# Optimization experiments

Measured on AMD Instinct MI355X. Metric: run time of the kernel, lower is better.

## Reference

```python
import jax, jax.numpy as jnp
import numpy as np

IN_SIZE = 1024
CLASSES = 7
N = 50000
LN_EPS = 1e-5


def _chain(x, w, b, g, beta):
    # Linear -> (Dropout=identity at eval) -> LayerNorm -> GELU(exact erf)
    h = x @ w.T + b
    mu = jnp.mean(h, axis=-1, keepdims=True)
    var = jnp.var(h, axis=-1, keepdims=True)
    h = (h - mu) / jnp.sqrt(var + LN_EPS) * g + beta
    return jax.nn.gelu(h, approximate=False)


def setup_inputs() -> dict:
    key = jax.random.key(0)
    ks = jax.random.split(key, 16)
    d = IN_SIZE
    std = 1.0 / np.sqrt(d)
    inp = {
        "features": jax.random.normal(ks[0], (N, d), jnp.float32),
        "c": jax.random.normal(ks[1], (N, CLASSES), jnp.float32),
        "key_w": jax.random.uniform(ks[2], (d, d), jnp.float32, -std, std),
        "key_b": jax.random.uniform(ks[3], (d,), jnp.float32, -std, std),
        "key_g": jnp.ones((d,), jnp.float32),
        "key_beta": jnp.zeros((d,), jnp.float32),
        "query_w": jax.random.uniform(ks[4], (d, d), jnp.float32, -std, std),
        "query_b": jax.random.uniform(ks[5], (d,), jnp.float32, -std, std),
        "query_g": jnp.ones((d,), jnp.float32),
        "query_beta": jnp.zeros((d,), jnp.float32),
        "value_w": jax.random.uniform(ks[6], (d, d), jnp.float32, -std, std),
        "value_b": jax.random.uniform(ks[7], (d,), jnp.float32, -std, std),
        "value_g": jnp.ones((d,), jnp.float32),
        "value_beta": jnp.zeros((d,), jnp.float32),
        "head_w": jax.random.uniform(ks[8], (CLASSES, CLASSES, d), jnp.float32, -1.0 / np.sqrt(CLASSES * d), 1.0 / np.sqrt(CLASSES * d)),
        "head_b": jax.random.uniform(ks[9], (CLASSES,), jnp.float32, -1.0 / np.sqrt(CLASSES * d), 1.0 / np.sqrt(CLASSES * d)),
    }
    return inp


def reference(features, c, key_w, key_b, key_g, key_beta,
              query_w, query_b, query_g, query_beta,
              value_w, value_b, value_g, value_beta,
              head_w, head_b):
    K = _chain(features, key_w, key_b, key_g, key_beta)          # [N, d]
    V = _chain(K, value_w, value_b, value_g, value_beta)         # [N, d]
    Q = _chain(K, query_w, query_b, query_g, query_beta)         # [N, d]
    # critical (top-scoring) instance per class
    top_idx = jnp.argmax(c, axis=0)                              # [classes]
    m_feats = K[top_idx]                                         # [classes, d]
    q_max = _chain(m_feats, query_w, query_b, query_g, query_beta)  # [classes, d]
    A = Q @ q_max.T                                              # [N, classes]
    A = jax.nn.softmax(A / jnp.sqrt(jnp.float32(Q.shape[1])), axis=0)
    B = A.T @ V                                                  # [classes, d]
    # Conv1d(classes, classes, kernel_size=d) on [1, classes, d] -> full contraction
    C = jnp.einsum('ik,oik->o', B, head_w) + head_b              # [classes]
    C = C.reshape(1, -1)
    return (C, A, B.reshape(1, CLASSES, -1))
```

## Files before the change

kernel.cpp:

```cpp
#include <hip/hip_runtime.h>


typedef unsigned short u16;
typedef __attribute__((ext_vector_type(8))) short          bf16x8;
typedef __attribute__((ext_vector_type(8))) unsigned short u16x8;
typedef __attribute__((ext_vector_type(4))) unsigned short u16x4;
typedef __attribute__((ext_vector_type(4))) float          f32x4;

#define DDIM  1024
#define NROWS 50000
#define MP    50048
#define NCLS  7
#define MPD4  12512

__device__ __forceinline__ u16 f2bf(float f) {
  unsigned u = __float_as_uint(f);
  u = (u + 0x7FFFu + ((u >> 16) & 1u)) >> 16;
  return (u16)u;
}
__device__ __forceinline__ float bf2f(u16 h) {
  return __uint_as_float(((unsigned)h) << 16);
}
__device__ __forceinline__ float gelu(float x) {
  return 0.5f * x * (1.0f + erff(x * 0.70710678118654752f));
}

__device__ __forceinline__ void load16_lds(const u16* g, u16* l) {
  __builtin_amdgcn_global_load_lds(
      (const __attribute__((address_space(1))) unsigned int*)(const void*)g,
      (__attribute__((address_space(3))) unsigned int*)(void*)l, 16, 0, 0);
}

__global__ __launch_bounds__(256) void k_convert(const float* __restrict__ src,
                                                 u16* __restrict__ dst,
                                                 int rows_total, int rows_valid) {
  const size_t total = (size_t)rows_total * DDIM / 8;
  const size_t stride = (size_t)gridDim.x * blockDim.x;
  for (size_t i = (size_t)blockIdx.x * blockDim.x + threadIdx.x; i < total; i += stride) {
    const size_t e = i * 8;
    const int row = (int)(e >> 10);
    u16x8 o = {0, 0, 0, 0, 0, 0, 0, 0};
    if (row < rows_valid) {
      const float4* p = (const float4*)(src + e);
      float4 f0 = p[0], f1 = p[1];
      o[0] = f2bf(f0.x); o[1] = f2bf(f0.y); o[2] = f2bf(f0.z); o[3] = f2bf(f0.w);
      o[4] = f2bf(f1.x); o[5] = f2bf(f1.y); o[6] = f2bf(f1.z); o[7] = f2bf(f1.w);
    }
    *(u16x8*)(dst + e) = o;
  }
}

__global__ __launch_bounds__(256) void k_convw(const float* __restrict__ kw,
                                               const float* __restrict__ vw,
                                               const float* __restrict__ qw,
                                               u16* __restrict__ Wk,
                                               u16* __restrict__ Wvq) {
  const int w = blockIdx.x >> 7;
  const int b = blockIdx.x & 127;
  const float* src = (w == 0) ? kw : (w == 1) ? vw : qw;
  u16* dst = (w == 0) ? Wk : (Wvq + (size_t)(w - 1) * DDIM * DDIM);
  for (int i = b * 256 + threadIdx.x; i < DDIM * DDIM / 8; i += 128 * 256) {
    const float4* p = (const float4*)(src + (size_t)i * 8);
    float4 f0 = p[0], f1 = p[1];
    u16x8 o;
    o[0] = f2bf(f0.x); o[1] = f2bf(f0.y); o[2] = f2bf(f0.z); o[3] = f2bf(f0.w);
    o[4] = f2bf(f1.x); o[5] = f2bf(f1.y); o[6] = f2bf(f1.z); o[7] = f2bf(f1.w);
    *(u16x8*)(dst + (size_t)i * 8) = o;
  }
}

__global__ __launch_bounds__(256) void k_gemm_bt(const u16* __restrict__ A,
                                                 const u16* __restrict__ B,
                                                 u16* __restrict__ C,
                                                 int lnn, int ldc) {
  __shared__ __align__(16) u16 As[4][4096];
  __shared__ __align__(16) u16 Bs[4][4096];
  const int tid  = threadIdx.x;
  const int lane = tid & 63;
  const int cpx = gridDim.x >> 3;
  const int v   = (blockIdx.x & 7) * cpx + (blockIdx.x >> 3);
  const int m0 = (v >> lnn) * 128;
  const int n0 = (v & ((1 << lnn) - 1)) * 128;
  const int wid = tid >> 6;
  const int wr = (wid >> 1) * 64;
  const int wc = (wid & 1) * 64;

  const int rA = tid >> 2;
  const int cA = (tid & 3) * 8;
  const u16* Ap0 = A + (size_t)(m0 + rA) * DDIM + cA;
  const u16* Ap1 = Ap0 + (size_t)64 * DDIM;
  const u16* Bp0 = B + (size_t)(n0 + rA) * DDIM + cA;
  const u16* Bp1 = Bp0 + (size_t)64 * DDIM;
  const int wb8 = wid * 512;

  f32x4 acc[4][4] = {};
  const int fr = lane & 15;
  const int kh = (lane >> 4) * 8;

#define STAGE_KT(KT) do { const int _b = (KT) & 3; const int _ko = (KT) * 32;  \
    load16_lds(Ap0 + _ko, &As[_b][wb8]);                                       \
    load16_lds(Ap1 + _ko, &As[_b][wb8 + 2048]);                                \
    load16_lds(Bp0 + _ko, &Bs[_b][wb8]);                                       \
    load16_lds(Bp1 + _ko, &Bs[_b][wb8 + 2048]); } while (0)

#define COMPUTE_KT(KT) do { const int _b = (KT) & 3;                           \
    const u16* _Ab = &As[_b][0]; const u16* _Bb = &Bs[_b][0];                  \
    bf16x8 a[4], b[4];                                                         \
    _Pragma("unroll") for (int i = 0; i < 4; ++i)                              \
      a[i] = *(const bf16x8*)&_Ab[(wr + i * 16 + fr) * 32 + kh];               \
    _Pragma("unroll") for (int j = 0; j < 4; ++j)                              \
      b[j] = *(const bf16x8*)&_Bb[(wc + j * 16 + fr) * 32 + kh];               \
    _Pragma("unroll") for (int i = 0; i < 4; ++i)                              \
      _Pragma("unroll") for (int j = 0; j < 4; ++j)                            \
        acc[i][j] = __builtin_amdgcn_mfma_f32_16x16x32_bf16(a[i], b[j],        \
                                                            acc[i][j], 0, 0, 0); } while (0)

  STAGE_KT(0); STAGE_KT(1); STAGE_KT(2);
  asm volatile("s_waitcnt vmcnt(8)\n\ts_barrier" ::: "memory");

#pragma unroll 4
  for (int kt = 0; kt < 28; ++kt) {
    STAGE_KT(kt + 3);
    COMPUTE_KT(kt);
    asm volatile("s_waitcnt vmcnt(8)\n\ts_barrier" ::: "memory");
  }
  STAGE_KT(31);
  COMPUTE_KT(28);
  asm volatile("s_waitcnt vmcnt(8)\n\ts_barrier" ::: "memory");
  COMPUTE_KT(29);
  asm volatile("s_waitcnt vmcnt(4)\n\ts_barrier" ::: "memory");
  COMPUTE_KT(30);
  asm volatile("s_waitcnt vmcnt(0)\n\ts_barrier" ::: "memory");
  COMPUTE_KT(31);
#undef STAGE_KT
#undef COMPUTE_KT

  const int orow = (lane >> 4) * 4;
  const int ocol = lane & 15;
#pragma unroll
  for (int i = 0; i < 4; ++i)
#pragma unroll
    for (int j = 0; j < 4; ++j) {
      const size_t base = (size_t)(m0 + wr + i * 16 + orow) * ldc + (n0 + wc + j * 16 + ocol);
#pragma unroll
      for (int r = 0; r < 4; ++r)
        C[base + (size_t)r * ldc] = f2bf(acc[i][j][r]);
    }
}

__global__ __launch_bounds__(256) void k_ln_k(const u16* __restrict__ h,
                                              const float* __restrict__ bias,
                                              const float* __restrict__ g,
                                              const float* __restrict__ beta,
                                              u16* __restrict__ out) {
  const int lane = threadIdx.x & 63;
  const int row = blockIdx.x * 4 + (threadIdx.x >> 6);
  const int c0 = lane * 8;
  u16x8* op0 = (u16x8*)(out + (size_t)row * DDIM + c0);
  u16x8* op1 = (u16x8*)(out + (size_t)row * DDIM + 512 + c0);
  if (row >= NROWS) {
    u16x8 z = {0, 0, 0, 0, 0, 0, 0, 0};
    *op0 = z; *op1 = z;
    return;
  }
  u16x8 h0 = *(const u16x8*)(h + (size_t)row * DDIM + c0);
  u16x8 h1 = *(const u16x8*)(h + (size_t)row * DDIM + 512 + c0);
  float4 a0 = *(const float4*)(bias + c0), a1 = *(const float4*)(bias + c0 + 4);
  float4 a2 = *(const float4*)(bias + 512 + c0), a3 = *(const float4*)(bias + 512 + c0 + 4);
  const float ba[8] = {a0.x, a0.y, a0.z, a0.w, a1.x, a1.y, a1.z, a1.w};
  const float bb[8] = {a2.x, a2.y, a2.z, a2.w, a3.x, a3.y, a3.z, a3.w};
  float v0[8], v1[8];
  float s1 = 0.f, s2 = 0.f;
#pragma unroll
  for (int e = 0; e < 8; ++e) {
    v0[e] = bf2f(h0[e]) + ba[e];
    v1[e] = bf2f(h1[e]) + bb[e];
    s1 += v0[e] + v1[e];
    s2 += v0[e] * v0[e] + v1[e] * v1[e];
  }
#pragma unroll
  for (int m = 1; m < 64; m <<= 1) {
    s1 += __shfl_xor(s1, m, 64);
    s2 += __shfl_xor(s2, m, 64);
  }
  const float mu = s1 * (1.0f / 1024.0f);
  const float var = s2 * (1.0f / 1024.0f) - mu * mu;
  const float rs = rsqrtf(var + 1e-5f);
  float4 g0 = *(const float4*)(g + c0), g1 = *(const float4*)(g + c0 + 4);
  float4 g2 = *(const float4*)(g + 512 + c0), g3 = *(const float4*)(g + 512 + c0 + 4);
  float4 t0 = *(const float4*)(beta + c0), t1 = *(const float4*)(beta + c0 + 4);
  float4 t2 = *(const float4*)(beta + 512 + c0), t3 = *(const float4*)(beta + 512 + c0 + 4);
  const float ga[8] = {g0.x, g0.y, g0.z, g0.w, g1.x, g1.y, g1.z, g1.w};
  const float gb[8] = {g2.x, g2.y, g2.z, g2.w, g3.x, g3.y, g3.z, g3.w};
  const float ta[8] = {t0.x, t0.y, t0.z, t0.w, t1.x, t1.y, t1.z, t1.w};
  const float tb[8] = {t2.x, t2.y, t2.z, t2.w, t3.x, t3.y, t3.z, t3.w};
  u16x8 o0, o1;
#pragma unroll
  for (int e = 0; e < 8; ++e) {
    o0[e] = f2bf(gelu((v0[e] - mu) * rs * ga[e] + ta[e]));
    o1[e] = f2bf(gelu((v1[e] - mu) * rs * gb[e] + tb[e]));
  }
  *op0 = o0; *op1 = o1;
}

__global__ __launch_bounds__(64) void k_qmax2(const float* __restrict__ argv,
                                              const int* __restrict__ argi,
                                              const u16* __restrict__ hvq,
                                              const float* __restrict__ qb,
                                              const float* __restrict__ qg,
                                              const float* __restrict__ qbeta,
                                              u16* __restrict__ qm) {
  const int j = blockIdx.x;
  const int lane = threadIdx.x;
  float bv = -3.4e38f; int bi = 0x7fffffff;
  for (int p = lane; p < 128; p += 64) {
    const float v = argv[p * NCLS + j];
    const int   i = argi[p * NCLS + j];
    if (v > bv || (v == bv && i < bi)) { bv = v; bi = i; }
  }
#pragma unroll
  for (int m = 1; m < 64; m <<= 1) {
    const float ov = __shfl_xor(bv, m, 64);
    const int   oi = __shfl_xor(bi, m, 64);
    if (ov > bv || (ov == bv && oi < bi)) { bv = ov; bi = oi; }
  }
  const int row = bi;
  const int c0 = lane * 8;
  const u16* hp = hvq + (size_t)row * 2048 + DDIM;
  u16x8 h0 = *(const u16x8*)(hp + c0);
  u16x8 h1 = *(const u16x8*)(hp + 512 + c0);
  float v0[8], v1[8];
  float s1 = 0.f, s2 = 0.f;
#pragma unroll
  for (int e = 0; e < 8; ++e) {
    v0[e] = bf2f(h0[e]) + qb[c0 + e];
    v1[e] = bf2f(h1[e]) + qb[512 + c0 + e];
    s1 += v0[e] + v1[e];
    s2 += v0[e] * v0[e] + v1[e] * v1[e];
  }
#pragma unroll
  for (int m = 1; m < 64; m <<= 1) {
    s1 += __shfl_xor(s1, m, 64);
    s2 += __shfl_xor(s2, m, 64);
  }
  const float mu = s1 * (1.0f / 1024.0f);
  const float var = s2 * (1.0f / 1024.0f) - mu * mu;
  const float rs = rsqrtf(var + 1e-5f);
  u16x8 o0, o1;
#pragma unroll
  for (int e = 0; e < 8; ++e) {
    o0[e] = f2bf(gelu((v0[e] - mu) * rs * qg[c0 + e] + qbeta[c0 + e]));
    o1[e] = f2bf(gelu((v1[e] - mu) * rs * qg[512 + c0 + e] + qbeta[512 + c0 + e]));
  }
  *(u16x8*)(qm + (size_t)j * DDIM + c0) = o0;
  *(u16x8*)(qm + (size_t)j * DDIM + 512 + c0) = o1;
}

__global__ __launch_bounds__(256) void k_ln_vq(const u16* __restrict__ h,
                                               const float* __restrict__ v_b,
                                               const float* __restrict__ v_g,
                                               const float* __restrict__ v_beta,
                                               const float* __restrict__ q_b,
                                               const float* __restrict__ q_g,
                                               const float* __restrict__ q_beta,
                                               const u16* __restrict__ qm,
                                               u16* __restrict__ V,
                                               float* __restrict__ logits) {
  __shared__ __align__(16) u16 sqm[NCLS * DDIM];
  const int tid = threadIdx.x;
  const int lane = tid & 63;
  const int half = (blockIdx.x >= MPD4) ? 1 : 0;
  const int rb = half ? (blockIdx.x - MPD4) : blockIdx.x;
  const int row = rb * 4 + (tid >> 6);
  if (half) {
    for (int i = tid; i < NCLS * DDIM / 8; i += 256)
      *(u16x8*)&sqm[i * 8] = *(const u16x8*)&qm[i * 8];
    __syncthreads();
  }
  if (row >= NROWS) return;
  const float* bias = half ? q_b : v_b;
  const float* gain = half ? q_g : v_g;
  const float* bet  = half ? q_beta : v_beta;
  const int c0 = lane * 8;
  const u16* hp = h + (size_t)row * 2048 + (size_t)half * DDIM;
  u16x8 h0 = *(const u16x8*)(hp + c0);
  u16x8 h1 = *(const u16x8*)(hp + 512 + c0);
  float4 a0 = *(const float4*)(bias + c0), a1 = *(const float4*)(bias + c0 + 4);
  float4 a2 = *(const float4*)(bias + 512 + c0), a3 = *(const float4*)(bias + 512 + c0 + 4);
  const float ba[8] = {a0.x, a0.y, a0.z, a0.w, a1.x, a1.y, a1.z, a1.w};
  const float bb[8] = {a2.x, a2.y, a2.z, a2.w, a3.x, a3.y, a3.z, a3.w};
  float v0[8], v1[8];
  float s1 = 0.f, s2 = 0.f;
#pragma unroll
  for (int e = 0; e < 8; ++e) {
    v0[e] = bf2f(h0[e]) + ba[e];
    v1[e] = bf2f(h1[e]) + bb[e];
    s1 += v0[e] + v1[e];
    s2 += v0[e] * v0[e] + v1[e] * v1[e];
  }
#pragma unroll
  for (int m = 1; m < 64; m <<= 1) {
    s1 += __shfl_xor(s1, m, 64);
    s2 += __shfl_xor(s2, m, 64);
  }
  const float mu = s1 * (1.0f / 1024.0f);
  const float var = s2 * (1.0f / 1024.0f) - mu * mu;
  const float rs = rsqrtf(var + 1e-5f);
  float4 g0 = *(const float4*)(gain + c0), g1 = *(const float4*)(gain + c0 + 4);
  float4 g2 = *(const float4*)(gain + 512 + c0), g3 = *(const float4*)(gain + 512 + c0 + 4);
  float4 t0 = *(const float4*)(bet + c0), t1 = *(const float4*)(bet + c0 + 4);
  float4 t2 = *(const float4*)(bet + 512 + c0), t3 = *(const float4*)(bet + 512 + c0 + 4);
  const float ga[8] = {g0.x, g0.y, g0.z, g0.w, g1.x, g1.y, g1.z, g1.w};
  const float gb[8] = {g2.x, g2.y, g2.z, g2.w, g3.x, g3.y, g3.z, g3.w};
  const float ta[8] = {t0.x, t0.y, t0.z, t0.w, t1.x, t1.y, t1.z, t1.w};
  const float tb[8] = {t2.x, t2.y, t2.z, t2.w, t3.x, t3.y, t3.z, t3.w};
  float y0[8], y1[8];
#pragma unroll
  for (int e = 0; e < 8; ++e) {
    y0[e] = gelu((v0[e] - mu) * rs * ga[e] + ta[e]);
    y1[e] = gelu((v1[e] - mu) * rs * gb[e] + tb[e]);
  }
  if (half == 0) {
    u16x8 o0, o1;
#pragma unroll
    for (int e = 0; e < 8; ++e) { o0[e] = f2bf(y0[e]); o1[e] = f2bf(y1[e]); }
    *(u16x8*)(V + (size_t)row * DDIM + c0) = o0;
    *(u16x8*)(V + (size_t)row * DDIM + 512 + c0) = o1;
  } else {
#pragma unroll
    for (int j = 0; j < NCLS; ++j) {
      u16x8 m0 = *(const u16x8*)&sqm[j * DDIM + c0];
      u16x8 m1 = *(const u16x8*)&sqm[j * DDIM + 512 + c0];
      float p = 0.f;
#pragma unroll
      for (int e = 0; e < 8; ++e) p += y0[e] * bf2f(m0[e]) + y1[e] * bf2f(m1[e]);
#pragma unroll
      for (int m = 1; m < 64; m <<= 1) p += __shfl_xor(p, m, 64);
      if (lane == 0) logits[(size_t)row * NCLS + j] = p * 0.03125f;
    }
  }
}

__global__ __launch_bounds__(256) void k_arg1(const float* __restrict__ c,
                                              float* __restrict__ pv,
                                              int* __restrict__ pi) {
  __shared__ float sv[256 * NCLS];
  __shared__ int   si[256 * NCLS];
  const int t = threadIdx.x;
  float bv[NCLS]; int bi[NCLS];
#pragma unroll
  for (int j = 0; j < NCLS; ++j) { bv[j] = -3.4e38f; bi[j] = 0x7fffffff; }
  for (int n = blockIdx.x * 256 + t; n < NROWS; n += 128 * 256) {
#pragma unroll
    for (int j = 0; j < NCLS; ++j) {
      const float v = c[(size_t)n * NCLS + j];
      if (v > bv[j]) { bv[j] = v; bi[j] = n; }
    }
  }
#pragma unroll
  for (int j = 0; j < NCLS; ++j) { sv[t * NCLS + j] = bv[j]; si[t * NCLS + j] = bi[j]; }
  __syncthreads();
  for (int s = 128; s > 0; s >>= 1) {
    if (t < s) {
#pragma unroll
      for (int j = 0; j < NCLS; ++j) {
        const float v2 = sv[(t + s) * NCLS + j]; const int i2 = si[(t + s) * NCLS + j];
        const float v1 = sv[t * NCLS + j];       const int i1 = si[t * NCLS + j];
        if (v2 > v1 || (v2 == v1 && i2 < i1)) { sv[t * NCLS + j] = v2; si[t * NCLS + j] = i2; }
      }
    }
    __syncthreads();
  }
  if (t < NCLS) { pv[blockIdx.x * NCLS + t] = sv[t]; pi[blockIdx.x * NCLS + t] = si[t]; }
}

__global__ __launch_bounds__(256) void k_cmax_part(const float* __restrict__ logits,
                                                   float* __restrict__ pout) {
  __shared__ float sm[256 * NCLS];
  const int tid = threadIdx.x;
  float m[NCLS];
#pragma unroll
  for (int j = 0; j < NCLS; ++j) m[j] = -3.4e38f;
  const size_t stride = (size_t)gridDim.x * 256;
  for (size_t n = (size_t)blockIdx.x * 256 + tid; n < NROWS; n += stride)
#pragma unroll
    for (int j = 0; j < NCLS; ++j) m[j] = fmaxf(m[j], logits[n * NCLS + j]);
#pragma unroll
  for (int j = 0; j < NCLS; ++j) sm[tid * NCLS + j] = m[j];
  __syncthreads();
  for (int s = 128; s > 0; s >>= 1) {
    if (tid < s)
#pragma unroll
      for (int j = 0; j < NCLS; ++j)
        sm[tid * NCLS + j] = fmaxf(sm[tid * NCLS + j], sm[(tid + s) * NCLS + j]);
    __syncthreads();
  }
  if (tid < NCLS) pout[blockIdx.x * NCLS + tid] = sm[tid];
}

__global__ __launch_bounds__(256) void k_csum_part(const float* __restrict__ logits,
                                                   const float* __restrict__ Pmax,
                                                   float* __restrict__ pout) {
  __shared__ float sm[256 * NCLS];
  __shared__ float sM[NCLS];
  const int tid = threadIdx.x;
  if (tid < NCLS) {
    float m = -3.4e38f;
    for (int b = 0; b < 128; ++b) m = fmaxf(m, Pmax[b * NCLS + tid]);
    sM[tid] = m;
  }
  __syncthreads();
  float s[NCLS];
#pragma unroll
  for (int j = 0; j < NCLS; ++j) s[j] = 0.f;
  const size_t stride = (size_t)gridDim.x * 256;
  for (size_t n = (size_t)blockIdx.x * 256 + tid; n < NROWS; n += stride)
#pragma unroll
    for (int j = 0; j < NCLS; ++j) s[j] += expf(logits[n * NCLS + j] - sM[j]);
#pragma unroll
  for (int j = 0; j < NCLS; ++j) sm[tid * NCLS + j] = s[j];
  __syncthreads();
  for (int st = 128; st > 0; st >>= 1) {
    if (tid < st)
#pragma unroll
      for (int j = 0; j < NCLS; ++j) sm[tid * NCLS + j] += sm[(tid + st) * NCLS + j];
    __syncthreads();
  }
  if (tid < NCLS) pout[blockIdx.x * NCLS + tid] = sm[tid];
}

__global__ __launch_bounds__(256) void k_bpart(const float* __restrict__ logits,
                                               const float* __restrict__ Pmax,
                                               const float* __restrict__ Psum,
                                               const u16* __restrict__ V,
                                               float* __restrict__ Aout,
                                               float* __restrict__ Pb) {
  __shared__ float sA[98 * NCLS];
  __shared__ float sM[NCLS], sR[NCLS];
  const int t = threadIdx.x;
  if (t < NCLS) {
    float m = -3.4e38f;
    for (int b = 0; b < 128; ++b) m = fmaxf(m, Pmax[b * NCLS + t]);
    float s = 0.f;
    for (int b = 0; b < 128; ++b) s += Psum[b * NCLS + t];
    sM[t] = m; sR[t] = 1.0f / s;
  }
  __syncthreads();
  const int n0 = blockIdx.x * 98;
  int cnt = NROWS - n0;
  cnt = cnt < 0 ? 0 : (cnt > 98 ? 98 : cnt);
  for (int idx = t; idx < cnt * NCLS; idx += 256) {
    const int j = idx % NCLS;
    const float a = expf(logits[(size_t)n0 * NCLS + idx] - sM[j]) * sR[j];
    sA[idx] = a;
    Aout[(size_t)n0 * NCLS + idx] = a;
  }
  __syncthreads();
  float acc[NCLS][4] = {};
  for (int r = 0; r < cnt; ++r) {
    u16x4 vv = *(const u16x4*)&V[(size_t)(n0 + r) * DDIM + t * 4];
    const float f0 = bf2f(vv[0]), f1 = bf2f(vv[1]), f2 = bf2f(vv[2]), f3 = bf2f(vv[3]);
#pragma unroll
    for (int j = 0; j < NCLS; ++j) {
      const float a = sA[r * NCLS + j];
      acc[j][0] += a * f0; acc[j][1] += a * f1; acc[j][2] += a * f2; acc[j][3] += a * f3;
    }
  }
#pragma unroll
  for (int j = 0; j < NCLS; ++j) {
    f32x4 o = {acc[j][0], acc[j][1], acc[j][2], acc[j][3]};
    *(f32x4*)&Pb[((size_t)blockIdx.x * NCLS + j) * DDIM + t * 4] = o;
  }
}

__global__ void k_bred(const float* __restrict__ Pb, float* __restrict__ Bout) {
  const int idx = blockIdx.x * 256 + threadIdx.x;
  if (idx >= NCLS * DDIM) return;
  float s = 0.f;
  for (int p = 0; p < 512; ++p) s += Pb[(size_t)p * NCLS * DDIM + idx];
  Bout[idx] = s;
}

__global__ __launch_bounds__(256) void k_head(const float* __restrict__ Bmat,
                                              const float* __restrict__ hw,
                                              const float* __restrict__ hb,
                                              float* __restrict__ Cout) {
  const int o = blockIdx.x, t = threadIdx.x;
  float p = 0.f;
  for (int idx = t; idx < NCLS * DDIM; idx += 256)
    p += Bmat[idx] * hw[(size_t)o * NCLS * DDIM + idx];
#pragma unroll
  for (int m = 1; m < 64; m <<= 1) p += __shfl_xor(p, m, 64);
  __shared__ float w[4];
  if ((t & 63) == 0) w[t >> 6] = p;
  __syncthreads();
  if (t == 0) Cout[o] = w[0] + w[1] + w[2] + w[3] + hb[o];
}

extern "C" void kernel_launch(void* const* d_in, const int* in_sizes, int n_in,
                              void* d_out, int out_size, void* d_ws, size_t ws_size,
                              hipStream_t stream) {
  const float* features   = (const float*)d_in[0];
  const float* c_in       = (const float*)d_in[1];
  const float* key_w      = (const float*)d_in[2];
  const float* key_b      = (const float*)d_in[3];
  const float* key_g      = (const float*)d_in[4];
  const float* key_beta   = (const float*)d_in[5];
  const float* query_w    = (const float*)d_in[6];
  const float* query_b    = (const float*)d_in[7];
  const float* query_g    = (const float*)d_in[8];
  const float* query_beta = (const float*)d_in[9];
  const float* value_w    = (const float*)d_in[10];
  const float* value_b    = (const float*)d_in[11];
  const float* value_g    = (const float*)d_in[12];
  const float* value_beta = (const float*)d_in[13];
  const float* head_w     = (const float*)d_in[14];
  const float* head_b     = (const float*)d_in[15];

  char* ws = (char*)d_ws;
  const size_t SZB = (size_t)MP * DDIM * 2;
  u16* Xb   = (u16*)ws;
  u16* HbVQ = Xb;
  u16* HbK  = (u16*)(ws + SZB);
  u16* Kb   = (u16*)(ws + 2 * SZB);
  u16* Vb   = Kb;
  size_t off = 3 * SZB;
  u16* Wk  = (u16*)(ws + off); off += (size_t)DDIM * DDIM * 2;
  u16* Wvq = (u16*)(ws + off); off += (size_t)2 * DDIM * DDIM * 2;
  float* logits = (float*)(ws + off); off += ((size_t)NROWS * NCLS * 4 + 255) & ~(size_t)255;
  float* Pb  = (float*)(ws + off); off += (size_t)512 * NCLS * DDIM * 4;
  u16* qm    = (u16*)(ws + off); off += ((size_t)NCLS * DDIM * 2 + 255) & ~(size_t)255;
  float* Pmax = (float*)(ws + off); off += ((size_t)128 * NCLS * 4 + 255) & ~(size_t)255;
  float* Psum = (float*)(ws + off); off += ((size_t)128 * NCLS * 4 + 255) & ~(size_t)255;
  float* argv = (float*)(ws + off); off += ((size_t)128 * NCLS * 4 + 255) & ~(size_t)255;
  int*   argi = (int*)  (ws + off); off += ((size_t)128 * NCLS * 4 + 255) & ~(size_t)255;

  float* Cout = (float*)d_out;
  float* Aout = Cout + NCLS;
  float* Bout = Aout + (size_t)NROWS * NCLS;

  k_arg1<<<128, 256, 0, stream>>>(c_in, argv, argi);
  k_convert<<<2048, 256, 0, stream>>>(features, Xb, MP, NROWS);
  k_convw<<<384, 256, 0, stream>>>(key_w, value_w, query_w, Wk, Wvq);

  k_gemm_bt<<<3128, 256, 0, stream>>>(Xb, Wk, HbK, 3, 1024);
  k_ln_k<<<MPD4, 256, 0, stream>>>(HbK, key_b, key_g, key_beta, Kb);

  k_gemm_bt<<<6256, 256, 0, stream>>>(Kb, Wvq, HbVQ, 4, 2048);
  k_qmax2<<<NCLS, 64, 0, stream>>>(argv, argi, HbVQ, query_b, query_g, query_beta, qm);
  k_ln_vq<<<2 * MPD4, 256, 0, stream>>>(HbVQ, value_b, value_g, value_beta,
                                        query_b, query_g, query_beta, qm, Vb, logits);

  k_cmax_part<<<128, 256, 0, stream>>>(logits, Pmax);
  k_csum_part<<<128, 256, 0, stream>>>(logits, Pmax, Psum);

  k_bpart<<<512, 256, 0, stream>>>(logits, Pmax, Psum, Vb, Aout, Pb);
  k_bred<<<28, 256, 0, stream>>>(Pb, Bout);
  k_head<<<NCLS, 256, 0, stream>>>(Bout, head_w, head_b, Cout);
}
```

Measured before the change: 823.7 us.

## Swizzle GEMM LDS layout and shrink prefetch ring to three stages

Applies an XOR swizzle to the k-chunk column of each row as it is written to and read from LDS, aiming to remove bank conflicts on the MFMA operand reads. It also cuts the LDS ring buffer from four stages to three, with an explicitly unrolled rotation of buffer indices. The smaller LDS footprint may allow more resident blocks per CU, but it leaves only one stage of prefetch lookahead, which could expose load latency.

```diff
diff --git a/kernel.cpp b/kernel.cpp
--- a/kernel.cpp
+++ b/kernel.cpp
@@ -73,8 +73,8 @@
                                                  const u16* __restrict__ B,
                                                  u16* __restrict__ C,
                                                  int lnn, int ldc) {
-  __shared__ __align__(16) u16 As[4][4096];
-  __shared__ __align__(16) u16 Bs[4][4096];
+  __shared__ __align__(16) u16 As[3][4096];
+  __shared__ __align__(16) u16 Bs[3][4096];
   const int tid  = threadIdx.x;
   const int lane = tid & 63;
   const int cpx = gridDim.x >> 3;
@@ -86,7 +86,7 @@
   const int wc = (wid & 1) * 64;
 
   const int rA = tid >> 2;
-  const int cA = (tid & 3) * 8;
+  const int cA = (((tid & 3) ^ ((rA >> 1) & 3)) << 3);
   const u16* Ap0 = A + (size_t)(m0 + rA) * DDIM + cA;
   const u16* Ap1 = Ap0 + (size_t)64 * DDIM;
   const u16* Bp0 = B + (size_t)(n0 + rA) * DDIM + cA;
@@ -95,45 +95,45 @@
 
   f32x4 acc[4][4] = {};
   const int fr = lane & 15;
-  const int kh = (lane >> 4) * 8;
-
-#define STAGE_KT(KT) do { const int _b = (KT) & 3; const int _ko = (KT) * 32;  \
-    load16_lds(Ap0 + _ko, &As[_b][wb8]);                                       \
-    load16_lds(Ap1 + _ko, &As[_b][wb8 + 2048]);                                \
-    load16_lds(Bp0 + _ko, &Bs[_b][wb8]);                                       \
-    load16_lds(Bp1 + _ko, &Bs[_b][wb8 + 2048]); } while (0)
-
-#define COMPUTE_KT(KT) do { const int _b = (KT) & 3;                           \
-    const u16* _Ab = &As[_b][0]; const u16* _Bb = &Bs[_b][0];                  \
+  const int T  = lane >> 4;
+
+#define STAGE_KT(KT, BUF) do { const int _ko = (KT) * 32;                      \
+    load16_lds(Ap0 + _ko, &As[BUF][wb8]);                                      \
+    load16_lds(Ap1 + _ko, &As[BUF][wb8 + 2048]);                               \
+    load16_lds(Bp0 + _ko, &Bs[BUF][wb8]);                                      \
+    load16_lds(Bp1 + _ko, &Bs[BUF][wb8 + 2048]); } while (0)
+
+#define COMPUTE_KT(BUF) do {                                                   \
+    const u16* _Ab = &As[BUF][0]; const u16* _Bb = &Bs[BUF][0];                \
     bf16x8 a[4], b[4];                                                         \
-    _Pragma("unroll") for (int i = 0; i < 4; ++i)                              \
-      a[i] = *(const bf16x8*)&_Ab[(wr + i * 16 + fr) * 32 + kh];               \
-    _Pragma("unroll") for (int j = 0; j < 4; ++j)                              \
-      b[j] = *(const bf16x8*)&_Bb[(wc + j * 16 + fr) * 32 + kh];               \
+    _Pragma("unroll") for (int i = 0; i < 4; ++i) {                            \
+      const int R = wr + i * 16 + fr;                                          \
+      a[i] = *(const bf16x8*)&_Ab[R * 32 + ((T ^ ((R >> 1) & 3)) << 3)];       \
+    }                                                                          \
+    _Pragma("unroll") for (int j = 0; j < 4; ++j) {                            \
+      const int R = wc + j * 16 + fr;                                          \
+      b[j] = *(const bf16x8*)&_Bb[R * 32 + ((T ^ ((R >> 1) & 3)) << 3)];       \
+    }                                                                          \
     _Pragma("unroll") for (int i = 0; i < 4; ++i)                              \
       _Pragma("unroll") for (int j = 0; j < 4; ++j)                            \
         acc[i][j] = __builtin_amdgcn_mfma_f32_16x16x32_bf16(a[i], b[j],        \
                                                             acc[i][j], 0, 0, 0); } while (0)
 
-  STAGE_KT(0); STAGE_KT(1); STAGE_KT(2);
-  asm volatile("s_waitcnt vmcnt(8)\n\ts_barrier" ::: "memory");
-
-#pragma unroll 4
-  for (int kt = 0; kt < 28; ++kt) {
-    STAGE_KT(kt + 3);
-    COMPUTE_KT(kt);
-    asm volatile("s_waitcnt vmcnt(8)\n\ts_barrier" ::: "memory");
-  }
-  STAGE_KT(31);
-  COMPUTE_KT(28);
-  asm volatile("s_waitcnt vmcnt(8)\n\ts_barrier" ::: "memory");
-  COMPUTE_KT(29);
-  asm volatile("s_waitcnt vmcnt(4)\n\ts_barrier" ::: "memory");
-  COMPUTE_KT(30);
-  asm volatile("s_waitcnt vmcnt(0)\n\ts_barrier" ::: "memory");
-  COMPUTE_KT(31);
+#define RBAR(N) asm volatile("s_waitcnt vmcnt(" #N ")\n\ts_barrier" ::: "memory")
+
+  STAGE_KT(0, 0); STAGE_KT(1, 1);
+  RBAR(4);
+  for (int kt = 0; kt < 30; kt += 3) {
+    STAGE_KT(kt + 2, 2); COMPUTE_KT(0); RBAR(4);
+    STAGE_KT(kt + 3, 0); COMPUTE_KT(1); RBAR(4);
+    STAGE_KT(kt + 4, 1); COMPUTE_KT(2); RBAR(4);
+  }
+  COMPUTE_KT(0);
+  RBAR(0);
+  COMPUTE_KT(1);
 #undef STAGE_KT
 #undef COMPUTE_KT
+#undef RBAR
 
   const int orow = (lane >> 4) * 4;
   const int ocol = lane & 15;
```

After: 826.7 us. No clear change (+0.4%).
